# Performance work log

Measured on AMD Instinct MI355X. Metric: run time of the kernel, lower is better.

Reference implementation:

```python
import jax, jax.numpy as jnp
import numpy as np

HEADS = 16
DIM_HEAD = 64
DIM = 1024
INNER = HEADS * DIM_HEAD  # 1024
DIM_OUT = 1024


def setup_inputs() -> dict:
    key = jax.random.key(0)
    k1, k2, k3, k4 = jax.random.split(key, 4)
    B, N = 4, 2048
    x = jax.random.normal(k1, (B, N, DIM), dtype=jnp.float32)
    # hk.Linear(inner_dim*3, with_bias=False): weight shape [in, out]
    w_qkv = jax.random.normal(k2, (DIM, INNER * 3), dtype=jnp.float32) / np.sqrt(DIM)
    # hk.Linear(dim_out): weight [INNER, DIM_OUT] + bias
    w_out = jax.random.normal(k3, (INNER, DIM_OUT), dtype=jnp.float32) / np.sqrt(INNER)
    b_out = jax.random.normal(k4, (DIM_OUT,), dtype=jnp.float32) * 0.01
    return {"x": x, "w_qkv": w_qkv, "w_out": w_out, "b_out": b_out}


def reference(x, w_qkv, w_out, b_out):
    B, N, _ = x.shape
    scale = DIM_HEAD ** -0.5
    qkv = x @ w_qkv  # [B, N, 3*INNER]
    q, k, v = jnp.split(qkv, 3, axis=-1)
    # b n (h d) -> b h n d
    split_heads = lambda t: t.reshape(B, N, HEADS, DIM_HEAD).transpose(0, 2, 1, 3)
    q, k, v = split_heads(q), split_heads(k), split_heads(v)
    dots = jnp.einsum('bhid,bhjd->bhij', q, k) * scale  # [B, H, N, N]
    attn = jax.nn.softmax(dots, axis=-1)
    out = jnp.einsum('bhij,bhjd->bhid', attn, v)  # [B, H, N, D]
    out = out.transpose(0, 2, 1, 3).reshape(B, N, INNER)  # b h n d -> b n (h d)
    return out @ w_out + b_out
```

## Files before the change

kernel.cpp:

```cpp
#include <hip/hip_runtime.h>
#include <cstdint>


typedef unsigned short ushort_t;
typedef _Float16 half_t;
typedef half_t half8 __attribute__((ext_vector_type(8)));
typedef half_t half4 __attribute__((ext_vector_type(4)));
typedef __fp16 fp16x2 __attribute__((ext_vector_type(2)));
typedef float floatx4 __attribute__((ext_vector_type(4)));

#define QSCALE 0.18033688011112043f

__device__ __forceinline__ float bf2f(ushort_t h) {
  union { unsigned int u; float f; } v; v.u = ((unsigned int)h) << 16; return v.f;
}
__device__ __forceinline__ void async_copy16(const void* g, void* l) {
  __builtin_amdgcn_global_load_lds(
      reinterpret_cast<const __attribute__((address_space(1))) unsigned int*>(
          reinterpret_cast<uintptr_t>(g)),
      reinterpret_cast<__attribute__((address_space(3))) unsigned int*>(
          reinterpret_cast<uintptr_t>(l)),
      16, 0, 0);
}
__device__ __forceinline__ void lds_fence() {
  asm volatile("s_waitcnt lgkmcnt(0)" ::: "memory");
}
__device__ __forceinline__ void vm_fence() {
  asm volatile("s_waitcnt vmcnt(0)" ::: "memory");
}

__global__ __launch_bounds__(256) void detect_dtype(const ushort_t* __restrict__ x,
                                                    int* __restrict__ flag) {
  __shared__ int cnt;
  if (threadIdx.x == 0) cnt = 0;
  __syncthreads();
  int local = 0;
  for (int i = threadIdx.x; i < 8192; i += 256)
    if ((x[i] & 0x7F80u) == 0x7F80u) ++local;
  atomicAdd(&cnt, local);
  __syncthreads();
  if (threadIdx.x == 0) *flag = (cnt >= 2) ? 1 : 0;
}

__global__ __launch_bounds__(256) void convert_to_f16(const void* __restrict__ src,
                                                      half_t* __restrict__ dst, int n,
                                                      const int* __restrict__ flag) {
  const int i0 = (blockIdx.x * 256 + threadIdx.x) * 4;
  if (i0 >= n) return;
  if (*flag) {
    const float* s = (const float*)src;
#pragma unroll
    for (int j = 0; j < 4; ++j) dst[i0 + j] = (half_t)s[i0 + j];
  } else {
    const ushort_t* s = (const ushort_t*)src;
#pragma unroll
    for (int j = 0; j < 4; ++j) dst[i0 + j] = (half_t)bf2f(s[i0 + j]);
  }
}

__global__ __launch_bounds__(256) void convert_bias(const void* __restrict__ src,
                                                    float* __restrict__ dst,
                                                    const int* __restrict__ flag) {
  const int i = blockIdx.x * 256 + threadIdx.x;
  if (i >= 1024) return;
  dst[i] = (*flag) ? ((const float*)src)[i] : bf2f(((const ushort_t*)src)[i]);
}

__global__ __launch_bounds__(256) void transpose_conv2(const void* __restrict__ srcA,
                                                       half_t* __restrict__ dstA,
                                                       const void* __restrict__ srcB,
                                                       half_t* __restrict__ dstB,
                                                       const int* __restrict__ flag) {
  __shared__ half_t tile[64][65];
  const int bx = blockIdx.x;
  const void* src; half_t* dst; int C, c0;
  if (bx < 48) { src = srcA; dst = dstA; C = 3072; c0 = bx * 64; }
  else         { src = srcB; dst = dstB; C = 1024; c0 = (bx - 48) * 64; }
  const int R = 1024;
  const int r0 = blockIdx.y * 64;
  const int tx = threadIdx.x & 63, ty = threadIdx.x >> 6;
  if (*flag) {
    const float* s = (const float*)src;
    for (int i = ty; i < 64; i += 4) tile[i][tx] = (half_t)s[(size_t)(r0 + i) * C + (c0 + tx)];
  } else {
    const ushort_t* s = (const ushort_t*)src;
    for (int i = ty; i < 64; i += 4) tile[i][tx] = (half_t)bf2f(s[(size_t)(r0 + i) * C + (c0 + tx)]);
  }
  __syncthreads();
  for (int i = ty; i < 64; i += 4) dst[(size_t)(c0 + i) * R + (r0 + tx)] = tile[tx][i];
}

__global__ __launch_bounds__(256) void gemm_qkv_kernel(
    const half_t* __restrict__ X, const half_t* __restrict__ WT,
    half_t* __restrict__ Qb, half_t* __restrict__ Kb, half_t* __restrict__ VTb) {
  __shared__ half_t smem[128 * 136];
  half_t* As = smem;
  half_t* Bs = smem + 128 * 64;
  const int tid = threadIdx.x;
  const int wv = tid >> 6, lane = tid & 63;
  const int l15 = lane & 15, quad = lane >> 4;
  const int l7 = l15 & 7;
  const int wm = wv & 1, wn = wv >> 1;
  const int bid = blockIdx.x;
  const int xcd = bid & 7, idx = bid >> 3;
  const int mb = xcd * 8 + (idx & 7);
  const int nb = idx >> 3;
  const int rlo = lane >> 3, ci = lane & 7;
  const int sw_klo = (ci ^ rlo) * 8;

  floatx4 acc[4][4];
  const floatx4 z = {0.f, 0.f, 0.f, 0.f};
#pragma unroll
  for (int mi = 0; mi < 4; ++mi)
#pragma unroll
    for (int ni = 0; ni < 4; ++ni) acc[mi][ni] = z;

  const half_t* Abase = X + (size_t)mb * 128 * 1024;
  const half_t* Bbase = WT + (size_t)nb * 128 * 1024;

  for (int k0 = 0; k0 < 1024; k0 += 64) {
#pragma unroll
    for (int j = 0; j < 4; ++j) {
      const int rb = (wv * 4 + j) * 8;
      async_copy16(Abase + (size_t)(rb + rlo) * 1024 + k0 + sw_klo, &As[rb * 64]);
    }
#pragma unroll
    for (int j = 0; j < 4; ++j) {
      const int rb = (wv * 4 + j) * 8;
      async_copy16(Bbase + (size_t)(rb + rlo) * 1024 + k0 + sw_klo, &Bs[rb * 64]);
    }
    __syncthreads();
#pragma unroll
    for (int ks = 0; ks < 2; ++ks) {
      half8 af[4], bfv[4];
#pragma unroll
      for (int mi = 0; mi < 4; ++mi) {
        const int rr = wm * 64 + mi * 16 + l15;
        af[mi] = *(const half8*)&As[rr * 64 + (((ks * 4 + quad) ^ l7) * 8)];
      }
#pragma unroll
      for (int ni = 0; ni < 4; ++ni) {
        const int rr = wn * 64 + ni * 16 + l15;
        bfv[ni] = *(const half8*)&Bs[rr * 64 + (((ks * 4 + quad) ^ l7) * 8)];
      }
#pragma unroll
      for (int mi = 0; mi < 4; ++mi)
#pragma unroll
        for (int ni = 0; ni < 4; ++ni)
          acc[mi][ni] = __builtin_amdgcn_mfma_f32_16x16x32_f16(af[mi], bfv[ni], acc[mi][ni], 0, 0, 0);
    }
    __syncthreads();
  }

  const int which = nb >> 3;
  if (which != 2) {
    const float sc = (which == 0) ? QSCALE : 1.0f;
#pragma unroll
    for (int mi = 0; mi < 4; ++mi)
#pragma unroll
      for (int ni = 0; ni < 4; ++ni) {
        const int col = wn * 64 + ni * 16 + l15;
#pragma unroll
        for (int r = 0; r < 4; ++r) {
          const int row = wm * 64 + mi * 16 + quad * 4 + r;
          smem[row * 132 + col] = (half_t)(acc[mi][ni][r] * sc);
        }
      }
    __syncthreads();
    half_t* dstB = (which == 0) ? Qb : Kb;
    const int hbase = (nb & 7) * 2;
    const int c2 = lane * 2;
    const int hh = hbase + (c2 >> 6);
    const int dd = c2 & 63;
#pragma unroll 4
    for (int i = 0; i < 32; ++i) {
      const int row = wv * 32 + i;
      const uint32_t val = *(const uint32_t*)&smem[row * 132 + c2];
      const int rowg = mb * 128 + row;
      const int bb = rowg >> 11, nn = rowg & 2047;
      *(uint32_t*)&dstB[(((size_t)(bb * 16 + hh)) * 2048 + nn) * 64 + dd] = val;
    }
  } else {
    const int nb2 = nb - 16;
#pragma unroll
    for (int mi = 0; mi < 4; ++mi)
#pragma unroll
      for (int ni = 0; ni < 4; ++ni) {
        const int nl = wn * 64 + ni * 16 + l15;
#pragma unroll
        for (int r = 0; r < 4; ++r) {
          const int ml = wm * 64 + mi * 16 + quad * 4 + r;
          smem[nl * 136 + ml] = (half_t)acc[mi][ni][r];
        }
      }
    __syncthreads();
    const int bb = mb >> 4;
    const int nn0 = (mb * 128) & 2047;
    const int lane2 = lane * 2;
#pragma unroll 4
    for (int it = 0; it < 32; ++it) {
      const int row = it * 4 + wv;
      const int hh = nb2 * 2 + (row >> 6);
      const int dd = row & 63;
      const int keyoff = lane2 ^ ((dd & 8) ? 4 : 0);
      const uint32_t val = *(const uint32_t*)&smem[row * 136 + lane2];
      *(uint32_t*)&VTb[((size_t)((bb * 16 + hh) * 64 + dd)) * 2048 + nn0 + keyoff] = val;
    }
  }
}

__global__ __launch_bounds__(256) void attn_kernel(
    const half_t* __restrict__ Qb, const half_t* __restrict__ Kb,
    const half_t* __restrict__ VTb, half_t* __restrict__ Ob) {
  __shared__ half_t smem[16384];
  const int tid = threadIdx.x, wv = tid >> 6, lane = tid & 63;
  const int l15 = lane & 15, quad = lane >> 4;
  const int l7 = l15 & 7;
  const int bid = blockIdx.x;
  const int xcd = bid & 7, idx = bid >> 3;
  const int bh = ((idx & 7) << 3) + xcd;
  const int qt = idx >> 3;
  const int bq = bh >> 4, hh = bh & 15;
  const half_t* Qg = Qb + (size_t)bh * 2048 * 64;
  const half_t* Kg = Kb + (size_t)bh * 2048 * 64;
  const half_t* Vg = VTb + (size_t)bh * 64 * 2048;
  const int q0 = qt * 128;
  const int rlo = lane >> 3, ci = lane & 7;
  const int sw_klo = (ci ^ rlo) * 8;

  const int q1 = quad >> 1, qb0 = quad & 1, b3 = (l15 >> 3) & 1;
  int kx[2], vx[4];
#pragma unroll
  for (int ks = 0; ks < 2; ++ks) kx[ks] = ((ks * 4 + quad) ^ l7) * 8;
#pragma unroll
  for (int ki = 0; ki < 4; ++ki)
    vx[ki] = (((ki * 2 + q1) ^ l7) * 8) + ((qb0 ^ b3) * 4);

#pragma unroll
  for (int j = 0; j < 4; ++j) {
    const int rb = (wv * 4 + j) * 8;
    async_copy16(Qg + (size_t)(q0 + rb + rlo) * 64 + sw_klo, &smem[rb * 64]);
  }
  vm_fence();
  half8 aq[2][2];
#pragma unroll
  for (int ks = 0; ks < 2; ++ks)
#pragma unroll
    for (int qi = 0; qi < 2; ++qi) {
      const int rr = wv * 32 + qi * 16 + l15;
      aq[ks][qi] = *(const half8*)&smem[rr * 64 + (((ks * 4 + quad) ^ l7) * 8)];
    }
  __syncthreads();

  floatx4 o_acc[2][4];
  const floatx4 z = {0.f, 0.f, 0.f, 0.f};
  float l_st[2] = {0.f, 0.f};
#pragma unroll
  for (int qi = 0; qi < 2; ++qi)
#pragma unroll
    for (int di = 0; di < 4; ++di) o_acc[qi][di] = z;

  {
#pragma unroll
    for (int j = 0; j < 2; ++j) {
      const int rb = (wv * 2 + j) * 8;
      async_copy16(Kg + (size_t)(rb + rlo) * 64 + sw_klo, &smem[rb * 64]);
    }
#pragma unroll
    for (int j = 0; j < 2; ++j) {
      const int db = (wv * 2 + j) * 8;
      async_copy16(Vg + (size_t)(db + rlo) * 2048 + sw_klo, &smem[8192 + db * 64]);
    }
  }

#pragma unroll 2
  for (int t = 0; t < 32; ++t) {
    const int co = (t & 1) * 4096;
    const int po = 4096 - co;
    __syncthreads();
    if (t < 31) {
#pragma unroll
      for (int j = 0; j < 2; ++j) {
        const int rb = (wv * 2 + j) * 8;
        async_copy16(Kg + (size_t)((t + 1) * 64 + rb + rlo) * 64 + sw_klo,
                     &smem[po + rb * 64]);
      }
#pragma unroll
      for (int j = 0; j < 2; ++j) {
        const int db = (wv * 2 + j) * 8;
        async_copy16(Vg + (size_t)(db + rlo) * 2048 + (t + 1) * 64 + sw_klo,
                     &smem[8192 + po + db * 64]);
      }
    }
    const half_t* Kc = &smem[co];
    const half_t* Vc = &smem[8192 + co];

    floatx4 s_acc[4][2];
#pragma unroll
    for (int ki = 0; ki < 4; ++ki)
#pragma unroll
      for (int qi = 0; qi < 2; ++qi) s_acc[ki][qi] = z;
#pragma unroll
    for (int ks = 0; ks < 2; ++ks) {
      half8 bk[4];
#pragma unroll
      for (int ki = 0; ki < 4; ++ki)
        bk[ki] = *(const half8*)&Kc[(ki * 16 + l15) * 64 + kx[ks]];
      __builtin_amdgcn_s_setprio(1);
#pragma unroll
      for (int ki = 0; ki < 4; ++ki)
#pragma unroll
        for (int qi = 0; qi < 2; ++qi)
          s_acc[ki][qi] = __builtin_amdgcn_mfma_f32_16x16x32_f16(bk[ki], aq[ks][qi], s_acc[ki][qi], 0, 0, 0);
      __builtin_amdgcn_s_setprio(0);
    }

    union Ap { uint32_t u[4]; half8 h; };
    Ap apu[2][2];
#pragma unroll
    for (int ki = 0; ki < 4; ++ki)
#pragma unroll
      for (int qi = 0; qi < 2; ++qi) {
        const float p0 = __builtin_amdgcn_exp2f(s_acc[ki][qi][0]);
        const float p1 = __builtin_amdgcn_exp2f(s_acc[ki][qi][1]);
        const float p2 = __builtin_amdgcn_exp2f(s_acc[ki][qi][2]);
        const float p3 = __builtin_amdgcn_exp2f(s_acc[ki][qi][3]);
        l_st[qi] += (p0 + p1) + (p2 + p3);
        union { fp16x2 v; uint32_t u; } lo_, hi_;
        lo_.v = __builtin_amdgcn_cvt_pkrtz(p0, p1);
        hi_.v = __builtin_amdgcn_cvt_pkrtz(p2, p3);
        apu[ki >> 1][qi].u[(ki & 1) * 2] = lo_.u;
        apu[ki >> 1][qi].u[(ki & 1) * 2 + 1] = hi_.u;
      }

#pragma unroll
    for (int c = 0; c < 2; ++c) {
      half8 bv[4];
#pragma unroll
      for (int di = 0; di < 4; ++di) {
        union { half4 q[2]; half8 v; } b_;
        b_.q[0] = *(const half4*)&Vc[(di * 16 + l15) * 64 + vx[2 * c]];
        b_.q[1] = *(const half4*)&Vc[(di * 16 + l15) * 64 + vx[2 * c + 1]];
        bv[di] = b_.v;
      }
      __builtin_amdgcn_s_setprio(1);
#pragma unroll
      for (int qi = 0; qi < 2; ++qi)
#pragma unroll
        for (int di = 0; di < 4; ++di)
          o_acc[qi][di] = __builtin_amdgcn_mfma_f32_16x16x32_f16(apu[c][qi].h, bv[di], o_acc[qi][di], 0, 0, 0);
      __builtin_amdgcn_s_setprio(0);
    }
  }

  float linv[2];
#pragma unroll
  for (int qi = 0; qi < 2; ++qi) {
    float rs = l_st[qi];
    rs += __shfl_xor(rs, 16);
    rs += __shfl_xor(rs, 32);
    linv[qi] = 1.0f / rs;
  }

  __syncthreads();
#pragma unroll
  for (int qi = 0; qi < 2; ++qi)
#pragma unroll
    for (int r = 0; r < 4; ++r) {
      const float inv = __shfl(linv[qi], quad * 4 + r);
      const int row = wv * 32 + qi * 16 + quad * 4 + r;
#pragma unroll
      for (int di = 0; di < 4; ++di)
        smem[row * 72 + di * 16 + l15] = (half_t)(o_acc[qi][di][r] * inv);
    }
  lds_fence();
  const int c2 = (lane & 31) * 2;
  const int rsel = lane >> 5;
#pragma unroll 4
  for (int i = 0; i < 16; ++i) {
    const int row = wv * 32 + i * 2 + rsel;
    const uint32_t val = *(const uint32_t*)&smem[row * 72 + c2];
    const int nn = q0 + row;
    *(uint32_t*)&Ob[((size_t)(bq * 2048 + nn)) * 1024 + hh * 64 + c2] = val;
  }
}

__global__ __launch_bounds__(256) void gemm_out_kernel(
    const half_t* __restrict__ A, const half_t* __restrict__ WT,
    const float* __restrict__ bias, float* __restrict__ out) {
  __shared__ half_t As[128 * 64];
  __shared__ half_t Bs[128 * 64];
  const int tid = threadIdx.x;
  const int wv = tid >> 6, lane = tid & 63;
  const int l15 = lane & 15, quad = lane >> 4;
  const int l7 = l15 & 7;
  const int wm = wv & 1, wn = wv >> 1;
  const int bid = blockIdx.x;
  const int xcd = bid & 7, idx = bid >> 3;
  const int mb = xcd * 8 + (idx & 7);
  const int nb = idx >> 3;
  const int rlo = lane >> 3, ci = lane & 7;
  const int sw_klo = (ci ^ rlo) * 8;

  floatx4 acc[4][4];
  const floatx4 z = {0.f, 0.f, 0.f, 0.f};
#pragma unroll
  for (int mi = 0; mi < 4; ++mi)
#pragma unroll
    for (int ni = 0; ni < 4; ++ni) acc[mi][ni] = z;

  const half_t* Abase = A + (size_t)mb * 128 * 1024;
  const half_t* Bbase = WT + (size_t)nb * 128 * 1024;

  for (int k0 = 0; k0 < 1024; k0 += 64) {
#pragma unroll
    for (int j = 0; j < 4; ++j) {
      const int rb = (wv * 4 + j) * 8;
      async_copy16(Abase + (size_t)(rb + rlo) * 1024 + k0 + sw_klo, &As[rb * 64]);
    }
#pragma unroll
    for (int j = 0; j < 4; ++j) {
      const int rb = (wv * 4 + j) * 8;
      async_copy16(Bbase + (size_t)(rb + rlo) * 1024 + k0 + sw_klo, &Bs[rb * 64]);
    }
    __syncthreads();
#pragma unroll
    for (int ks = 0; ks < 2; ++ks) {
      half8 af[4], bfv[4];
#pragma unroll
      for (int mi = 0; mi < 4; ++mi) {
        const int rr = wm * 64 + mi * 16 + l15;
        af[mi] = *(const half8*)&As[rr * 64 + (((ks * 4 + quad) ^ l7) * 8)];
      }
#pragma unroll
      for (int ni = 0; ni < 4; ++ni) {
        const int rr = wn * 64 + ni * 16 + l15;
        bfv[ni] = *(const half8*)&Bs[rr * 64 + (((ks * 4 + quad) ^ l7) * 8)];
      }
#pragma unroll
      for (int mi = 0; mi < 4; ++mi)
#pragma unroll
        for (int ni = 0; ni < 4; ++ni)
          acc[mi][ni] = __builtin_amdgcn_mfma_f32_16x16x32_f16(af[mi], bfv[ni], acc[mi][ni], 0, 0, 0);
    }
    __syncthreads();
  }

#pragma unroll
  for (int mi = 0; mi < 4; ++mi) {
#pragma unroll
    for (int ni = 0; ni < 4; ++ni) {
      const int colg = nb * 128 + wn * 64 + ni * 16 + l15;
      const float bs = bias[colg];
#pragma unroll
      for (int r = 0; r < 4; ++r) {
        const int rowg = mb * 128 + wm * 64 + mi * 16 + quad * 4 + r;
        out[(size_t)rowg * 1024 + colg] = acc[mi][ni][r] + bs;
      }
    }
  }
}

extern "C" void kernel_launch(void* const* d_in, const int* in_sizes, int n_in,
                              void* d_out, int out_size, void* d_ws, size_t ws_size,
                              hipStream_t stream) {
  const void* x_raw     = d_in[0];
  const void* w_qkv_raw = d_in[1];
  const void* w_out_raw = d_in[2];
  const void* b_out_raw = d_in[3];
  float* out = (float*)d_out;

  char* ws = (char*)d_ws;
  half_t* xb    = (half_t*)(ws);
  half_t* Qb    = (half_t*)(ws + ((size_t)16 << 20));
  half_t* Kb    = (half_t*)(ws + ((size_t)32 << 20));
  half_t* VTb   = (half_t*)(ws + ((size_t)48 << 20));
  half_t* WTqkv = (half_t*)(ws + ((size_t)64 << 20));
  half_t* WTout = (half_t*)(ws + ((size_t)70 << 20));
  float*  bb    = (float*)(ws + ((size_t)72 << 20));
  int*    flag  = (int*)(ws + ((size_t)72 << 20) + 8192);
  half_t* Ob    = xb;

  detect_dtype<<<1, 256, 0, stream>>>((const ushort_t*)x_raw, flag);
  convert_to_f16<<<8192, 256, 0, stream>>>(x_raw, xb, 8192 * 1024, flag);
  convert_bias<<<4, 256, 0, stream>>>(b_out_raw, bb, flag);
  transpose_conv2<<<dim3(64, 16), 256, 0, stream>>>(w_qkv_raw, WTqkv, w_out_raw, WTout, flag);
  gemm_qkv_kernel<<<1536, 256, 0, stream>>>(xb, WTqkv, Qb, Kb, VTb);
  attn_kernel<<<1024, 256, 0, stream>>>(Qb, Kb, VTb, Ob);
  gemm_out_kernel<<<512, 256, 0, stream>>>(Ob, WTout, bb, out);
}
```

Baseline: 290.1 us.

## Split attention key tile into halves and stagger KV start per block

The inner attention loop now handles each 64-key tile as two 32-key groups. Each group does its QK MFMAs, exp2 and PV MFMAs in turn, so exponentials of one group can overlap matrix work of another and fewer score registers are live. Separately, blocks start their KV sweep at a rotated tile offset derived from the block index, which spreads concurrent blocks across different K/V addresses to reduce L2/HBM channel contention. The rotation is valid only because the softmax here has no max-subtraction and is order-independent. The change alters the instruction schedule and register pressure, with some risk of different compiler behaviour.

```diff
diff --git a/kernel.cpp b/kernel.cpp
--- a/kernel.cpp
+++ b/kernel.cpp
@@ -221,6 +221,7 @@
   const int bh = ((idx & 7) << 3) + xcd;
   const int qt = idx >> 3;
   const int bq = bh >> 4, hh = bh & 15;
+  const int ph = ((idx >> 5) & 3) * 8;
   const half_t* Qg = Qb + (size_t)bh * 2048 * 64;
   const half_t* Kg = Kb + (size_t)bh * 2048 * 64;
   const half_t* Vg = VTb + (size_t)bh * 64 * 2048;
@@ -264,12 +265,12 @@
 #pragma unroll
     for (int j = 0; j < 2; ++j) {
       const int rb = (wv * 2 + j) * 8;
-      async_copy16(Kg + (size_t)(rb + rlo) * 64 + sw_klo, &smem[rb * 64]);
+      async_copy16(Kg + (size_t)(ph * 64 + rb + rlo) * 64 + sw_klo, &smem[rb * 64]);
     }
 #pragma unroll
     for (int j = 0; j < 2; ++j) {
       const int db = (wv * 2 + j) * 8;
-      async_copy16(Vg + (size_t)(db + rlo) * 2048 + sw_klo, &smem[8192 + db * 64]);
+      async_copy16(Vg + (size_t)(db + rlo) * 2048 + ph * 64 + sw_klo, &smem[8192 + db * 64]);
     }
   }
 
@@ -279,76 +280,77 @@
     const int po = 4096 - co;
     __syncthreads();
     if (t < 31) {
+      const int tp = (t + ph + 1) & 31;
 #pragma unroll
       for (int j = 0; j < 2; ++j) {
         const int rb = (wv * 2 + j) * 8;
-        async_copy16(Kg + (size_t)((t + 1) * 64 + rb + rlo) * 64 + sw_klo,
+        async_copy16(Kg + (size_t)(tp * 64 + rb + rlo) * 64 + sw_klo,
                      &smem[po + rb * 64]);
       }
 #pragma unroll
       for (int j = 0; j < 2; ++j) {
         const int db = (wv * 2 + j) * 8;
-        async_copy16(Vg + (size_t)(db + rlo) * 2048 + (t + 1) * 64 + sw_klo,
+        async_copy16(Vg + (size_t)(db + rlo) * 2048 + tp * 64 + sw_klo,
                      &smem[8192 + po + db * 64]);
       }
     }
     const half_t* Kc = &smem[co];
     const half_t* Vc = &smem[8192 + co];
 
-    floatx4 s_acc[4][2];
-#pragma unroll
-    for (int ki = 0; ki < 4; ++ki)
-#pragma unroll
-      for (int qi = 0; qi < 2; ++qi) s_acc[ki][qi] = z;
-#pragma unroll
-    for (int ks = 0; ks < 2; ++ks) {
-      half8 bk[4];
-#pragma unroll
-      for (int ki = 0; ki < 4; ++ki)
-        bk[ki] = *(const half8*)&Kc[(ki * 16 + l15) * 64 + kx[ks]];
+#pragma unroll
+    for (int g = 0; g < 2; ++g) {
+      floatx4 sA[2][2];
+#pragma unroll
+      for (int kii = 0; kii < 2; ++kii)
+#pragma unroll
+        for (int qi = 0; qi < 2; ++qi) sA[kii][qi] = z;
+      half8 bk[2][2];
+#pragma unroll
+      for (int ks = 0; ks < 2; ++ks)
+#pragma unroll
+        for (int kii = 0; kii < 2; ++kii)
+          bk[ks][kii] = *(const half8*)&Kc[((g * 2 + kii) * 16 + l15) * 64 + kx[ks]];
       __builtin_amdgcn_s_setprio(1);
 #pragma unroll
-      for (int ki = 0; ki < 4; ++ki)
-#pragma unroll
-        for (int qi = 0; qi < 2; ++qi)
-          s_acc[ki][qi] = __builtin_amdgcn_mfma_f32_16x16x32_f16(bk[ki], aq[ks][qi], s_acc[ki][qi], 0, 0, 0);
+      for (int ks = 0; ks < 2; ++ks)
+#pragma unroll
+        for (int kii = 0; kii < 2; ++kii)
+#pragma unroll
+          for (int qi = 0; qi < 2; ++qi)
+            sA[kii][qi] = __builtin_amdgcn_mfma_f32_16x16x32_f16(bk[ks][kii], aq[ks][qi], sA[kii][qi], 0, 0, 0);
       __builtin_amdgcn_s_setprio(0);
-    }
-
-    union Ap { uint32_t u[4]; half8 h; };
-    Ap apu[2][2];
-#pragma unroll
-    for (int ki = 0; ki < 4; ++ki)
-#pragma unroll
-      for (int qi = 0; qi < 2; ++qi) {
-        const float p0 = __builtin_amdgcn_exp2f(s_acc[ki][qi][0]);
-        const float p1 = __builtin_amdgcn_exp2f(s_acc[ki][qi][1]);
-        const float p2 = __builtin_amdgcn_exp2f(s_acc[ki][qi][2]);
-        const float p3 = __builtin_amdgcn_exp2f(s_acc[ki][qi][3]);
-        l_st[qi] += (p0 + p1) + (p2 + p3);
-        union { fp16x2 v; uint32_t u; } lo_, hi_;
-        lo_.v = __builtin_amdgcn_cvt_pkrtz(p0, p1);
-        hi_.v = __builtin_amdgcn_cvt_pkrtz(p2, p3);
-        apu[ki >> 1][qi].u[(ki & 1) * 2] = lo_.u;
-        apu[ki >> 1][qi].u[(ki & 1) * 2 + 1] = hi_.u;
-      }
-
-#pragma unroll
-    for (int c = 0; c < 2; ++c) {
+
       half8 bv[4];
 #pragma unroll
       for (int di = 0; di < 4; ++di) {
         union { half4 q[2]; half8 v; } b_;
-        b_.q[0] = *(const half4*)&Vc[(di * 16 + l15) * 64 + vx[2 * c]];
-        b_.q[1] = *(const half4*)&Vc[(di * 16 + l15) * 64 + vx[2 * c + 1]];
+        b_.q[0] = *(const half4*)&Vc[(di * 16 + l15) * 64 + vx[g * 2]];
+        b_.q[1] = *(const half4*)&Vc[(di * 16 + l15) * 64 + vx[g * 2 + 1]];
         bv[di] = b_.v;
       }
+
+      union Ap { uint32_t u[4]; half8 h; } apu[2];
+#pragma unroll
+      for (int kii = 0; kii < 2; ++kii)
+#pragma unroll
+        for (int qi = 0; qi < 2; ++qi) {
+          const float p0 = __builtin_amdgcn_exp2f(sA[kii][qi][0]);
+          const float p1 = __builtin_amdgcn_exp2f(sA[kii][qi][1]);
+          const float p2 = __builtin_amdgcn_exp2f(sA[kii][qi][2]);
+          const float p3 = __builtin_amdgcn_exp2f(sA[kii][qi][3]);
+          l_st[qi] += (p0 + p1) + (p2 + p3);
+          union { fp16x2 v; uint32_t u; } lo_, hi_;
+          lo_.v = __builtin_amdgcn_cvt_pkrtz(p0, p1);
+          hi_.v = __builtin_amdgcn_cvt_pkrtz(p2, p3);
+          apu[qi].u[kii * 2] = lo_.u;
+          apu[qi].u[kii * 2 + 1] = hi_.u;
+        }
       __builtin_amdgcn_s_setprio(1);
 #pragma unroll
       for (int qi = 0; qi < 2; ++qi)
 #pragma unroll
         for (int di = 0; di < 4; ++di)
-          o_acc[qi][di] = __builtin_amdgcn_mfma_f32_16x16x32_f16(apu[c][qi].h, bv[di], o_acc[qi][di], 0, 0, 0);
+          o_acc[qi][di] = __builtin_amdgcn_mfma_f32_16x16x32_f16(apu[qi].h, bv[di], o_acc[qi][di], 0, 0, 0);
       __builtin_amdgcn_s_setprio(0);
     }
   }
```

New measurement: 287.3 us. No clear change (-1.0%).

## Double attention query tile to 256 rows with 512-thread blocks sharing K/V

Applied to the files above, without the earlier changes.

Each attention block now has 8 waves and covers 256 query rows instead of 128, so every K/V tile staged in shared memory serves twice as many queries and the grid is halved. The K/V prefetch is split so each wave copies one 8-row slice. The output epilogue is reworked into two phases that reuse the same shared staging buffer, with extra barriers. The aim is to cut global and L2 K/V traffic per query. The cost is larger blocks, which may reduce scheduling flexibility and occupancy, plus the added synchronization in the epilogue.

```diff
diff --git a/kernel.cpp b/kernel.cpp
--- a/kernel.cpp
+++ b/kernel.cpp
@@ -209,7 +209,7 @@
   }
 }
 
-__global__ __launch_bounds__(256) void attn_kernel(
+__global__ __launch_bounds__(512) void attn_kernel(
     const half_t* __restrict__ Qb, const half_t* __restrict__ Kb,
     const half_t* __restrict__ VTb, half_t* __restrict__ Ob) {
   __shared__ half_t smem[16384];
@@ -224,7 +224,7 @@
   const half_t* Qg = Qb + (size_t)bh * 2048 * 64;
   const half_t* Kg = Kb + (size_t)bh * 2048 * 64;
   const half_t* Vg = VTb + (size_t)bh * 64 * 2048;
-  const int q0 = qt * 128;
+  const int q0 = qt * 256;
   const int rlo = lane >> 3, ci = lane & 7;
   const int sw_klo = (ci ^ rlo) * 8;
 
@@ -261,16 +261,9 @@
     for (int di = 0; di < 4; ++di) o_acc[qi][di] = z;
 
   {
-#pragma unroll
-    for (int j = 0; j < 2; ++j) {
-      const int rb = (wv * 2 + j) * 8;
-      async_copy16(Kg + (size_t)(rb + rlo) * 64 + sw_klo, &smem[rb * 64]);
-    }
-#pragma unroll
-    for (int j = 0; j < 2; ++j) {
-      const int db = (wv * 2 + j) * 8;
-      async_copy16(Vg + (size_t)(db + rlo) * 2048 + sw_klo, &smem[8192 + db * 64]);
-    }
+    const int rb = wv * 8;
+    async_copy16(Kg + (size_t)(rb + rlo) * 64 + sw_klo, &smem[rb * 64]);
+    async_copy16(Vg + (size_t)(rb + rlo) * 2048 + sw_klo, &smem[8192 + rb * 64]);
   }
 
 #pragma unroll 2
@@ -279,18 +272,11 @@
     const int po = 4096 - co;
     __syncthreads();
     if (t < 31) {
-#pragma unroll
-      for (int j = 0; j < 2; ++j) {
-        const int rb = (wv * 2 + j) * 8;
-        async_copy16(Kg + (size_t)((t + 1) * 64 + rb + rlo) * 64 + sw_klo,
-                     &smem[po + rb * 64]);
-      }
-#pragma unroll
-      for (int j = 0; j < 2; ++j) {
-        const int db = (wv * 2 + j) * 8;
-        async_copy16(Vg + (size_t)(db + rlo) * 2048 + (t + 1) * 64 + sw_klo,
-                     &smem[8192 + po + db * 64]);
-      }
+      const int rb = wv * 8;
+      async_copy16(Kg + (size_t)((t + 1) * 64 + rb + rlo) * 64 + sw_klo,
+                   &smem[po + rb * 64]);
+      async_copy16(Vg + (size_t)(rb + rlo) * 2048 + (t + 1) * 64 + sw_klo,
+                   &smem[8192 + po + rb * 64]);
     }
     const half_t* Kc = &smem[co];
     const half_t* Vc = &smem[8192 + co];
@@ -363,25 +349,32 @@
   }
 
   __syncthreads();
-#pragma unroll
-  for (int qi = 0; qi < 2; ++qi)
-#pragma unroll
-    for (int r = 0; r < 4; ++r) {
-      const float inv = __shfl(linv[qi], quad * 4 + r);
-      const int row = wv * 32 + qi * 16 + quad * 4 + r;
-#pragma unroll
-      for (int di = 0; di < 4; ++di)
-        smem[row * 72 + di * 16 + l15] = (half_t)(o_acc[qi][di][r] * inv);
-    }
-  lds_fence();
-  const int c2 = (lane & 31) * 2;
-  const int rsel = lane >> 5;
+  const int c2 = (tid & 31) * 2;
+  const int rbase = (tid >> 5) & 15;
+#pragma unroll
+  for (int p = 0; p < 2; ++p) {
+    if ((wv >> 2) == p) {
+      const int rw = (wv & 3) * 32;
+#pragma unroll
+      for (int qi = 0; qi < 2; ++qi)
+#pragma unroll
+        for (int r = 0; r < 4; ++r) {
+          const float inv = __shfl(linv[qi], quad * 4 + r);
+          const int rowl = rw + qi * 16 + quad * 4 + r;
+#pragma unroll
+          for (int di = 0; di < 4; ++di)
+            smem[rowl * 72 + di * 16 + l15] = (half_t)(o_acc[qi][di][r] * inv);
+        }
+    }
+    __syncthreads();
 #pragma unroll 4
-  for (int i = 0; i < 16; ++i) {
-    const int row = wv * 32 + i * 2 + rsel;
-    const uint32_t val = *(const uint32_t*)&smem[row * 72 + c2];
-    const int nn = q0 + row;
-    *(uint32_t*)&Ob[((size_t)(bq * 2048 + nn)) * 1024 + hh * 64 + c2] = val;
+    for (int i = 0; i < 8; ++i) {
+      const int rowl = i * 16 + rbase;
+      const uint32_t val = *(const uint32_t*)&smem[rowl * 72 + c2];
+      const int nn = q0 + p * 128 + rowl;
+      *(uint32_t*)&Ob[((size_t)(bq * 2048 + nn)) * 1024 + hh * 64 + c2] = val;
+    }
+    __syncthreads();
   }
 }
 
@@ -486,6 +479,6 @@
   convert_bias<<<4, 256, 0, stream>>>(b_out_raw, bb, flag);
   transpose_conv2<<<dim3(64, 16), 256, 0, stream>>>(w_qkv_raw, WTqkv, w_out_raw, WTout, flag);
   gemm_qkv_kernel<<<1536, 256, 0, stream>>>(xb, WTqkv, Qb, Kb, VTb);
-  attn_kernel<<<1024, 256, 0, stream>>>(Qb, Kb, VTb, Ob);
+  attn_kernel<<<512, 512, 0, stream>>>(Qb, Kb, VTb, Ob);
   gemm_out_kernel<<<512, 256, 0, stream>>>(Ob, WTout, bb, out);
 }
```

After: 269.6 us. 7.1% less time.
